# Performance work log

Hardware: AMD Instinct MI355X
Metric: run time of the kernel (lower is better)

The kernel has to match this reference:

```python
import jax, jax.numpy as jnp
import numpy as np

NUM_USERS = 200000
NUM_ITEMS = 100000
EMB = 64
NUM_LAYERS = 3


def setup_inputs() -> dict:
    rng = np.random.default_rng(0)
    E_INTER = 2_000_000
    # unique (user, item) interactions -> faithful to adj[e0, e1] = 1.0 set-semantics
    lin = np.unique(rng.integers(0, NUM_USERS * NUM_ITEMS, size=E_INTER, dtype=np.int64))
    u = (lin // NUM_ITEMS).astype(np.int32)
    it = (lin % NUM_ITEMS).astype(np.int32) + NUM_USERS  # item node ids offset by NUM_USERS
    row = np.concatenate([u, it])  # symmetric bipartite graph, no self-loops
    col = np.concatenate([it, u])
    edge_index = jnp.asarray(np.stack([row, col]), dtype=jnp.int32)  # [2, E]

    key = jax.random.key(0)
    k1, k2 = jax.random.split(key)
    # xavier_uniform on nn.Embedding.weight
    bu = float(np.sqrt(6.0 / (NUM_USERS + EMB)))
    bi = float(np.sqrt(6.0 / (NUM_ITEMS + EMB)))
    user_emb = jax.random.uniform(k1, (NUM_USERS, EMB), jnp.float32, -bu, bu)
    item_emb = jax.random.uniform(k2, (NUM_ITEMS, EMB), jnp.float32, -bi, bi)
    return {"edge_index": edge_index, "user_emb": user_emb, "item_emb": item_emb}


def reference(edge_index, user_emb, item_emb):
    num_users = user_emb.shape[0]
    N = num_users + item_emb.shape[0]
    x = jnp.concatenate([user_emb, item_emb], axis=0)  # ego embeddings [N, D]
    row, col = edge_index[0], edge_index[1]

    # adj has unique off-diagonal edges + eye(N): row-sum degree = edge count + 1
    deg = jax.ops.segment_sum(jnp.ones(row.shape, x.dtype), row, num_segments=N) + 1.0
    dinv = jax.lax.rsqrt(deg)                 # deg >= 1, never inf
    w = (dinv[row] * dinv[col])[:, None]      # per-edge D^-1/2 A D^-1/2 weight
    self_w = (dinv * dinv)[:, None]           # self-loop weight d_i^-1

    acc = x  # sum over layer outputs, including layer 0
    for _ in range(NUM_LAYERS):
        x = jax.ops.segment_sum(w * x[col], row, num_segments=N) + self_w * x
        # dropout is identity in eval mode
        acc = acc + x

    return acc[:num_users], acc[num_users:]
```

## Files before the change

### kernel.cpp

```cpp
#include <hip/hip_runtime.h>
#include <hip/hip_bf16.h>

#define EMB 64
#define BKT_BITS 10
#define BKT_SZ   (1 << BKT_BITS)
#define NBMAX    256
#define PAD      32
#define U_BITS   18
#define U_MASK   ((1u << U_BITS) - 1u)

__device__ __forceinline__ float bf2f(unsigned short h) {
    return __uint_as_float(((unsigned)h) << 16);
}
__device__ __forceinline__ unsigned short f2bf(float f) {
    unsigned u = __float_as_uint(f);
    unsigned r = (u + 0x7fffu + ((u >> 16) & 1u)) >> 16;
    return (unsigned short)r;
}

__global__ void k1_kernel(const int* __restrict__ row, const int* __restrict__ colh,
                          int* __restrict__ urp, float* __restrict__ dinv,
                          const float* __restrict__ ue, unsigned short* __restrict__ y0,
                          int* __restrict__ btotp,
                          int NU, int Eh, int NB, int UB) {
    __shared__ int bound[17];
    __shared__ int hist[NBMAX];
    int t = threadIdx.x;
    if ((int)blockIdx.x < UB) {
        int r0 = blockIdx.x * 16;
        if (t < 17) {
            int r = r0 + t;
            if (r <= NU) {
                int lo = 0, hi = Eh;
                while (lo < hi) {
                    int mid = (lo + hi) >> 1;
                    if (row[mid] < r) lo = mid + 1; else hi = mid;
                }
                bound[t] = lo;
                urp[r] = lo;
                if (t < 16 && r < NU)
                    dinv[r] = rsqrtf((float)(0) + 0.0f);
            }
        }
        __syncthreads();
        if (t < 16 && r0 + t < NU)
            dinv[r0 + t] = rsqrtf((float)(bound[t + 1] - bound[t]) + 1.0f);
        long j4 = (long)r0 * 64 + t * 4;
        if (j4 < (long)NU * 64) {
            int rb = t >> 4;
            float sc = rsqrtf((float)(bound[rb + 1] - bound[rb]) + 1.0f);
            float4 v = ((const float4*)ue)[j4 >> 2];
            ushort4 o;
            o.x = f2bf(sc * v.x); o.y = f2bf(sc * v.y);
            o.z = f2bf(sc * v.z); o.w = f2bf(sc * v.w);
            ((ushort4*)y0)[j4 >> 2] = o;
        }
    } else {
        hist[t] = 0;
        if (t + 256 < NBMAX) hist[t + 256] = 0;
        __syncthreads();
        long e0 = (long)(blockIdx.x - UB) * 4096;
#pragma unroll
        for (int k = 0; k < 16; ++k) {
            long e = e0 + k * 256 + t;
            if (e < Eh) atomicAdd(&hist[(colh[e] - NU) >> BKT_BITS], 1);
        }
        __syncthreads();
        if (t < NB && hist[t]) atomicAdd(&btotp[t * PAD], hist[t]);
    }
}

__global__ void scanS_kernel(const int* __restrict__ btotp, int* __restrict__ bbase,
                             int* __restrict__ bcurp, int NB, int Eh) {
    __shared__ int sh[256];
    int t = threadIdx.x;
    int v = (t < NB) ? btotp[t * PAD] : 0;
    sh[t] = v;
    __syncthreads();
    for (int off = 1; off < 256; off <<= 1) {
        int u = (t >= off) ? sh[t - off] : 0;
        __syncthreads();
        sh[t] += u;
        __syncthreads();
    }
    if (t < NB) {
        int excl = sh[t] - v;
        bbase[t] = excl;
        bcurp[t * PAD] = excl;
        if (t == NB - 1) bbase[NB] = sh[t];
    }
}

__global__ void passA_kernel(const int* __restrict__ rowh, const int* __restrict__ colh,
                             int* __restrict__ bcurp, unsigned* __restrict__ staging,
                             int Eh, int NU, int NB) {
    __shared__ int cnt[NBMAX];
    __shared__ int base[NBMAX];
    int t = threadIdx.x;
    cnt[t] = 0;
    if (t + 256 < NBMAX) cnt[t + 256] = 0;
    __syncthreads();
    long cb = (long)blockIdx.x * 1024;
    int b[4], rk[4];
    unsigned pk[4];
#pragma unroll
    for (int j = 0; j < 4; ++j) {
        long e = cb + j * 256 + t;
        if (e < Eh) {
            int u = rowh[e];
            int loc = colh[e] - NU;
            b[j] = loc >> BKT_BITS;
            pk[j] = ((unsigned)(loc & (BKT_SZ - 1)) << U_BITS) | (unsigned)u;
            rk[j] = atomicAdd(&cnt[b[j]], 1);
        } else {
            b[j] = -1;
        }
    }
    __syncthreads();
    if (t < NB) base[t] = cnt[t] ? atomicAdd(&bcurp[t * PAD], cnt[t]) : 0;
    __syncthreads();
#pragma unroll
    for (int j = 0; j < 4; ++j)
        if (b[j] >= 0) staging[base[b[j]] + rk[j]] = pk[j];
}

__global__ void passB_kernel(const unsigned* __restrict__ staging,
                             const int* __restrict__ bbase,
                             int* __restrict__ irp, int* __restrict__ icols,
                             float* __restrict__ dinv,
                             const float* __restrict__ ie, unsigned short* __restrict__ y0,
                             int NU, int NI, int NB, int Eh) {
    __shared__ int cnt[BKT_SZ];
    __shared__ int sh[BKT_SZ];
    int t = threadIdx.x;
    int b = blockIdx.x;
    int lo = b << BKT_BITS;
    int sb = bbase[b], se = bbase[b + 1];

    cnt[t] = 0;
    __syncthreads();
    for (int k = sb + t; k < se; k += 1024)
        atomicAdd(&cnt[staging[k] >> U_BITS], 1);
    __syncthreads();

    sh[t] = cnt[t];
    __syncthreads();
    for (int off = 1; off < 1024; off <<= 1) {
        int v = (t >= off) ? sh[t - off] : 0;
        __syncthreads();
        sh[t] += v;
        __syncthreads();
    }
    int exclv = sh[t] - cnt[t];
    int item = lo + t;
    if (item < NI) {
        irp[item] = sb + exclv;
        dinv[NU + item] = rsqrtf((float)cnt[t] + 1.0f);
    }
    if (b == NB - 1 && t == 0) irp[NI] = Eh;
    __syncthreads();
    sh[t] = exclv;
    __syncthreads();
    for (int k = sb + t; k < se; k += 1024) {
        unsigned v = staging[k];
        int io = (int)(v >> U_BITS);
        int r = atomicAdd(&sh[io], 1);
        icols[sb + r] = (int)(v & U_MASK);
    }

    for (int m = t; m < BKT_SZ * 16; m += 1024) {
        int it = lo + (m >> 4);
        if (it >= NI) break;
        float sc = rsqrtf((float)cnt[m >> 4] + 1.0f);
        float4 v = ((const float4*)ie)[(long)it * 16 + (m & 15)];
        ushort4 o;
        o.x = f2bf(sc * v.x); o.y = f2bf(sc * v.y);
        o.z = f2bf(sc * v.z); o.w = f2bf(sc * v.w);
        ((ushort4*)y0)[((long)NU + it) * 16 + (m & 15)] = o;
    }
}

__global__ void ul0_kernel(const int* __restrict__ urp, const int* __restrict__ colg,
                           const float* __restrict__ dinv,
                           const unsigned short* __restrict__ y0,
                           unsigned short* __restrict__ y1, int NU) {
    long t = (long)blockIdx.x * blockDim.x + threadIdx.x;
    int i = (int)(t >> 4);
    if (i >= NU) return;
    int q = (int)(t & 15);
    int s = urp[i], e = urp[i + 1];
    float di = dinv[i];
    const ushort4* __restrict__ y04 = (const ushort4*)y0;
    long p = (long)i * 16 + q;
    ushort4 sv = y04[p];

    float ax = 0.f, ay = 0.f, az = 0.f, aw = 0.f;
    for (int k0 = s; k0 < e; k0 += 8) {
        int   c[8];
        float w[8];
#pragma unroll
        for (int j = 0; j < 8; ++j) {
            int k = k0 + j;
            bool v = (k < e);
            c[j] = v ? colg[k] : 0;
            w[j] = v ? 1.0f : 0.0f;
        }
        ushort4 u[8];
#pragma unroll
        for (int j = 0; j < 8; ++j) u[j] = y04[(long)c[j] * 16 + q];
#pragma unroll
        for (int j = 0; j < 8; ++j) {
            ax += w[j] * bf2f(u[j].x);
            ay += w[j] * bf2f(u[j].y);
            az += w[j] * bf2f(u[j].z);
            aw += w[j] * bf2f(u[j].w);
        }
    }
    ax += bf2f(sv.x); ay += bf2f(sv.y); az += bf2f(sv.z); aw += bf2f(sv.w);
    float sq = di * di;
    ushort4 o;
    o.x = f2bf(sq * ax); o.y = f2bf(sq * ay); o.z = f2bf(sq * az); o.w = f2bf(sq * aw);
    ((ushort4*)y1)[p] = o;
}

__global__ void d2_kernel(const int* __restrict__ irp, const int* __restrict__ icols,
                          const float* __restrict__ dinv,
                          const unsigned short* __restrict__ y0,
                          unsigned short* __restrict__ y1,
                          unsigned short* __restrict__ y2, int NU, int NI) {
    long t = (long)blockIdx.x * blockDim.x + threadIdx.x;
    int j = (int)(t >> 4);
    if (j >= NI) return;
    int q = (int)(t & 15);
    int i = NU + j;
    int s = irp[j], e = irp[j + 1];
    float di = dinv[i];
    const ushort4* __restrict__ y04 = (const ushort4*)y0;
    const ushort4* __restrict__ y14 = (const ushort4*)y1;
    long p = (long)i * 16 + q;
    ushort4 sv0 = y04[p];

    float a0x = 0.f, a0y = 0.f, a0z = 0.f, a0w = 0.f;
    float a1x = 0.f, a1y = 0.f, a1z = 0.f, a1w = 0.f;
    for (int k0 = s; k0 < e; k0 += 8) {
        long  off[8];
        float w[8];
#pragma unroll
        for (int jj = 0; jj < 8; ++jj) {
            int k = k0 + jj;
            bool v = (k < e);
            int c = v ? icols[k] : 0;
            off[jj] = (long)c * 16 + q;
            w[jj] = v ? 1.0f : 0.0f;
        }
        ushort4 u0[8], u1[8];
#pragma unroll
        for (int jj = 0; jj < 8; ++jj) { u0[jj] = y04[off[jj]]; u1[jj] = y14[off[jj]]; }
#pragma unroll
        for (int jj = 0; jj < 8; ++jj) {
            a0x += w[jj] * bf2f(u0[jj].x); a0y += w[jj] * bf2f(u0[jj].y);
            a0z += w[jj] * bf2f(u0[jj].z); a0w += w[jj] * bf2f(u0[jj].w);
            a1x += w[jj] * bf2f(u1[jj].x); a1y += w[jj] * bf2f(u1[jj].y);
            a1z += w[jj] * bf2f(u1[jj].z); a1w += w[jj] * bf2f(u1[jj].w);
        }
    }
    float sq = di * di;
    a0x += bf2f(sv0.x); a0y += bf2f(sv0.y); a0z += bf2f(sv0.z); a0w += bf2f(sv0.w);
    ushort4 o1;
    o1.x = f2bf(sq * a0x); o1.y = f2bf(sq * a0y);
    o1.z = f2bf(sq * a0z); o1.w = f2bf(sq * a0w);
    ((ushort4*)y1)[p] = o1;
    a1x += bf2f(o1.x); a1y += bf2f(o1.y); a1z += bf2f(o1.z); a1w += bf2f(o1.w);
    ushort4 o2;
    o2.x = f2bf(sq * a1x); o2.y = f2bf(sq * a1y);
    o2.z = f2bf(sq * a1z); o2.w = f2bf(sq * a1w);
    ((ushort4*)y2)[p] = o2;
}

__global__ void d3_kernel(const int* __restrict__ urp, const int* __restrict__ colg,
                          const float* __restrict__ dinv,
                          const unsigned short* __restrict__ y0,
                          const unsigned short* __restrict__ y1,
                          unsigned short* __restrict__ y2,
                          float* __restrict__ out, int NU) {
    long t = (long)blockIdx.x * blockDim.x + threadIdx.x;
    int i = (int)(t >> 4);
    if (i >= NU) return;
    int q = (int)(t & 15);
    int s = urp[i], e = urp[i + 1];
    float di = dinv[i];
    const ushort4* __restrict__ y04 = (const ushort4*)y0;
    const ushort4* __restrict__ y14 = (const ushort4*)y1;
    const ushort4* __restrict__ y24 = (const ushort4*)y2;
    long p = (long)i * 16 + q;
    ushort4 sv0 = y04[p];
    ushort4 sv1 = y14[p];

    float a1x = 0.f, a1y = 0.f, a1z = 0.f, a1w = 0.f;
    float a2x = 0.f, a2y = 0.f, a2z = 0.f, a2w = 0.f;
    for (int k0 = s; k0 < e; k0 += 8) {
        long  off[8];
        float w[8];
#pragma unroll
        for (int jj = 0; jj < 8; ++jj) {
            int k = k0 + jj;
            bool v = (k < e);
            int c = v ? colg[k] : 0;
            off[jj] = (long)c * 16 + q;
            w[jj] = v ? 1.0f : 0.0f;
        }
        ushort4 u1[8], u2[8];
#pragma unroll
        for (int jj = 0; jj < 8; ++jj) { u1[jj] = y14[off[jj]]; u2[jj] = y24[off[jj]]; }
#pragma unroll
        for (int jj = 0; jj < 8; ++jj) {
            a1x += w[jj] * bf2f(u1[jj].x); a1y += w[jj] * bf2f(u1[jj].y);
            a1z += w[jj] * bf2f(u1[jj].z); a1w += w[jj] * bf2f(u1[jj].w);
            a2x += w[jj] * bf2f(u2[jj].x); a2y += w[jj] * bf2f(u2[jj].y);
            a2z += w[jj] * bf2f(u2[jj].z); a2w += w[jj] * bf2f(u2[jj].w);
        }
    }
    float sq = di * di;
    a1x += bf2f(sv1.x); a1y += bf2f(sv1.y); a1z += bf2f(sv1.z); a1w += bf2f(sv1.w);
    ushort4 o2;
    o2.x = f2bf(sq * a1x); o2.y = f2bf(sq * a1y);
    o2.z = f2bf(sq * a1z); o2.w = f2bf(sq * a1w);
    ((ushort4*)y2)[p] = o2;
    a2x += bf2f(o2.x); a2y += bf2f(o2.y); a2z += bf2f(o2.z); a2w += bf2f(o2.w);
    float inv = 1.0f / di;
    float4 o;
    o.x = (bf2f(sv0.x) + bf2f(sv1.x) + bf2f(o2.x)) * inv + di * a2x;
    o.y = (bf2f(sv0.y) + bf2f(sv1.y) + bf2f(o2.y)) * inv + di * a2y;
    o.z = (bf2f(sv0.z) + bf2f(sv1.z) + bf2f(o2.z)) * inv + di * a2z;
    o.w = (bf2f(sv0.w) + bf2f(sv1.w) + bf2f(o2.w)) * inv + di * a2w;
    ((float4*)out)[p] = o;
}

__global__ void d4_kernel(const int* __restrict__ irp, const int* __restrict__ icols,
                          const float* __restrict__ dinv,
                          const unsigned short* __restrict__ y0,
                          const unsigned short* __restrict__ y1,
                          const unsigned short* __restrict__ y2,
                          float* __restrict__ out, int NU, int NI) {
    long t = (long)blockIdx.x * blockDim.x + threadIdx.x;
    int j = (int)(t >> 4);
    if (j >= NI) return;
    int q = (int)(t & 15);
    int i = NU + j;
    int s = irp[j], e = irp[j + 1];
    float di = dinv[i];
    const ushort4* __restrict__ y04 = (const ushort4*)y0;
    const ushort4* __restrict__ y14 = (const ushort4*)y1;
    const ushort4* __restrict__ y24 = (const ushort4*)y2;
    long p = (long)i * 16 + q;
    ushort4 sv0 = y04[p];
    ushort4 sv1 = y14[p];
    ushort4 sv2 = y24[p];

    float ax = 0.f, ay = 0.f, az = 0.f, aw = 0.f;
    for (int k0 = s; k0 < e; k0 += 8) {
        int   c[8];
        float w[8];
#pragma unroll
        for (int jj = 0; jj < 8; ++jj) {
            int k = k0 + jj;
            bool v = (k < e);
            c[jj] = v ? icols[k] : 0;
            w[jj] = v ? 1.0f : 0.0f;
        }
        ushort4 u[8];
#pragma unroll
        for (int jj = 0; jj < 8; ++jj) u[jj] = y24[(long)c[jj] * 16 + q];
#pragma unroll
        for (int jj = 0; jj < 8; ++jj) {
            ax += w[jj] * bf2f(u[jj].x);
            ay += w[jj] * bf2f(u[jj].y);
            az += w[jj] * bf2f(u[jj].z);
            aw += w[jj] * bf2f(u[jj].w);
        }
    }
    ax += bf2f(sv2.x); ay += bf2f(sv2.y); az += bf2f(sv2.z); aw += bf2f(sv2.w);
    float inv = 1.0f / di;
    float4 o;
    o.x = (bf2f(sv0.x) + bf2f(sv1.x) + bf2f(sv2.x)) * inv + di * ax;
    o.y = (bf2f(sv0.y) + bf2f(sv1.y) + bf2f(sv2.y)) * inv + di * ay;
    o.z = (bf2f(sv0.z) + bf2f(sv1.z) + bf2f(sv2.z)) * inv + di * az;
    o.w = (bf2f(sv0.w) + bf2f(sv1.w) + bf2f(sv2.w)) * inv + di * aw;
    ((float4*)out)[p] = o;
}

extern "C" void kernel_launch(void* const* d_in, const int* in_sizes, int n_in,
                              void* d_out, int out_size, void* d_ws, size_t ws_size,
                              hipStream_t stream) {
    const int*   edge_index = (const int*)d_in[0];
    const float* user_emb   = (const float*)d_in[1];
    const float* item_emb   = (const float*)d_in[2];
    float* out = (float*)d_out;

    const int  E  = in_sizes[0] / 2;
    const int  Eh = E / 2;
    const int  NU = in_sizes[1] / EMB;
    const int  NI = in_sizes[2] / EMB;
    const int  N  = NU + NI;
    const long total = (long)N * EMB;

    const int* row = edge_index;
    const int* col = edge_index + E;
    const int* rowh = row;
    const int* colh = col;

    int*   urp   = (int*)d_ws;
    int*   btotp = urp + (NU + 1);
    int*   bcurp = btotp + NBMAX * PAD;
    int*   bbase = bcurp + NBMAX * PAD;
    int*   irp   = bbase + (NBMAX + 1);
    int*   icols = irp + (NI + 1);
    float* dinv  = (float*)(icols + Eh);
    unsigned short* y0 = (unsigned short*)(((uintptr_t)(dinv + N) + 127) & ~(uintptr_t)127);
    unsigned short* y1 = y0 + total;
    unsigned short* y2 = y1 + total;
    unsigned* staging = (unsigned*)(y1 + (long)NU * EMB);

    const int NB = (NI + BKT_SZ - 1) >> BKT_BITS;

    hipMemsetAsync(btotp, 0, (size_t)NBMAX * PAD * sizeof(int), stream);

    int UB = (NU + 15) / 16;
    int PC = (Eh + 4095) / 4096;
    k1_kernel<<<UB + PC, 256, 0, stream>>>(row, colh, urp, dinv, user_emb, y0,
                                           btotp, NU, Eh, NB, UB);

    scanS_kernel<<<1, 256, 0, stream>>>(btotp, bbase, bcurp, NB, Eh);

    passA_kernel<<<(Eh + 1023) / 1024, 256, 0, stream>>>(rowh, colh, bcurp, staging,
                                                         Eh, NU, NB);

    passB_kernel<<<NB, 1024, 0, stream>>>(staging, bbase, irp, icols, dinv,
                                          item_emb, y0, NU, NI, NB, Eh);

    int nb_us = (int)(((long)NU * 16 + 255) / 256);
    ul0_kernel<<<nb_us, 256, 0, stream>>>(urp, col, dinv, y0, y1, NU);

    int nb_it = (int)(((long)NI * 16 + 255) / 256);
    d2_kernel<<<nb_it, 256, 0, stream>>>(irp, icols, dinv, y0, y1, y2, NU, NI);

    d3_kernel<<<nb_us, 256, 0, stream>>>(urp, col, dinv, y0, y1, y2, out, NU);

    d4_kernel<<<nb_it, 256, 0, stream>>>(irp, icols, dinv, y0, y1, y2, out, NU, NI);
}
```

Measured before the change: 531.9 us.

## Interleave paired layer embeddings so each neighbor gather fetches one 16-byte vector

Changes the bf16 embedding buffers to an interleaved layout. User layer-0 and layer-1 rows are stored side by side, and so are item layer-1 and layer-2 rows. The d2 and d3 gathers can then fetch both needed layers for a neighbor with one uint4 load instead of two separate 8-byte loads. The aim is fewer gather transactions and better cache-line use in the memory-bound sparse aggregation. The cost is more complex indexing, and the layer-0 user writes and layer-1 reads now use strided half-lines.

```diff
diff --git a/kernel.cpp b/kernel.cpp
--- a/kernel.cpp
+++ b/kernel.cpp
@@ -17,10 +17,15 @@
     unsigned r = (u + 0x7fffu + ((u >> 16) & 1u)) >> 16;
     return (unsigned short)r;
 }
+__device__ __forceinline__ float bflo(unsigned p) { return __uint_as_float(p << 16); }
+__device__ __forceinline__ float bfhi(unsigned p) { return __uint_as_float(p & 0xffff0000u); }
+__device__ __forceinline__ unsigned pack2(float a, float b) {
+    return (unsigned)f2bf(a) | ((unsigned)f2bf(b) << 16);
+}
 
 __global__ void k1_kernel(const int* __restrict__ row, const int* __restrict__ colh,
                           int* __restrict__ urp, float* __restrict__ dinv,
-                          const float* __restrict__ ue, unsigned short* __restrict__ y0,
+                          const float* __restrict__ ue, unsigned short* __restrict__ yu01,
                           int* __restrict__ btotp,
                           int NU, int Eh, int NB, int UB) {
     __shared__ int bound[17];
@@ -38,8 +43,6 @@
                 }
                 bound[t] = lo;
                 urp[r] = lo;
-                if (t < 16 && r < NU)
-                    dinv[r] = rsqrtf((float)(0) + 0.0f);
             }
         }
         __syncthreads();
@@ -48,16 +51,16 @@
         long j4 = (long)r0 * 64 + t * 4;
         if (j4 < (long)NU * 64) {
             int rb = t >> 4;
+            int q  = t & 15;
             float sc = rsqrtf((float)(bound[rb + 1] - bound[rb]) + 1.0f);
             float4 v = ((const float4*)ue)[j4 >> 2];
             ushort4 o;
             o.x = f2bf(sc * v.x); o.y = f2bf(sc * v.y);
             o.z = f2bf(sc * v.z); o.w = f2bf(sc * v.w);
-            ((ushort4*)y0)[j4 >> 2] = o;
+            ((ushort4*)yu01)[((long)(r0 + rb) * 16 + q) * 2 + 0] = o;
         }
     } else {
         hist[t] = 0;
-        if (t + 256 < NBMAX) hist[t + 256] = 0;
         __syncthreads();
         long e0 = (long)(blockIdx.x - UB) * 4096;
 #pragma unroll
@@ -98,7 +101,6 @@
     __shared__ int base[NBMAX];
     int t = threadIdx.x;
     cnt[t] = 0;
-    if (t + 256 < NBMAX) cnt[t + 256] = 0;
     __syncthreads();
     long cb = (long)blockIdx.x * 1024;
     int b[4], rk[4];
@@ -128,7 +130,7 @@
                              const int* __restrict__ bbase,
                              int* __restrict__ irp, int* __restrict__ icols,
                              float* __restrict__ dinv,
-                             const float* __restrict__ ie, unsigned short* __restrict__ y0,
+                             const float* __restrict__ ie, unsigned short* __restrict__ y0i,
                              int NU, int NI, int NB, int Eh) {
     __shared__ int cnt[BKT_SZ];
     __shared__ int sh[BKT_SZ];
@@ -176,23 +178,22 @@
         ushort4 o;
         o.x = f2bf(sc * v.x); o.y = f2bf(sc * v.y);
         o.z = f2bf(sc * v.z); o.w = f2bf(sc * v.w);
-        ((ushort4*)y0)[((long)NU + it) * 16 + (m & 15)] = o;
+        ((ushort4*)y0i)[(long)it * 16 + (m & 15)] = o;
     }
 }
 
 __global__ void ul0_kernel(const int* __restrict__ urp, const int* __restrict__ colg,
                            const float* __restrict__ dinv,
-                           const unsigned short* __restrict__ y0,
-                           unsigned short* __restrict__ y1, int NU) {
+                           const unsigned short* __restrict__ y0i,
+                           unsigned short* __restrict__ yu01, int NU) {
     long t = (long)blockIdx.x * blockDim.x + threadIdx.x;
     int i = (int)(t >> 4);
     if (i >= NU) return;
     int q = (int)(t & 15);
     int s = urp[i], e = urp[i + 1];
     float di = dinv[i];
-    const ushort4* __restrict__ y04 = (const ushort4*)y0;
-    long p = (long)i * 16 + q;
-    ushort4 sv = y04[p];
+    const ushort4* __restrict__ y0is = (const ushort4*)y0i - (long)NU * 16;
+    ushort4 sv = ((const ushort4*)yu01)[((long)i * 16 + q) * 2 + 0];
 
     float ax = 0.f, ay = 0.f, az = 0.f, aw = 0.f;
     for (int k0 = s; k0 < e; k0 += 8) {
@@ -202,12 +203,12 @@
         for (int j = 0; j < 8; ++j) {
             int k = k0 + j;
             bool v = (k < e);
-            c[j] = v ? colg[k] : 0;
+            c[j] = v ? colg[k] : NU;
             w[j] = v ? 1.0f : 0.0f;
         }
         ushort4 u[8];
 #pragma unroll
-        for (int j = 0; j < 8; ++j) u[j] = y04[(long)c[j] * 16 + q];
+        for (int j = 0; j < 8; ++j) u[j] = y0is[(long)c[j] * 16 + q];
 #pragma unroll
         for (int j = 0; j < 8; ++j) {
             ax += w[j] * bf2f(u[j].x);
@@ -220,68 +221,63 @@
     float sq = di * di;
     ushort4 o;
     o.x = f2bf(sq * ax); o.y = f2bf(sq * ay); o.z = f2bf(sq * az); o.w = f2bf(sq * aw);
-    ((ushort4*)y1)[p] = o;
+    ((ushort4*)yu01)[((long)i * 16 + q) * 2 + 1] = o;
 }
 
 __global__ void d2_kernel(const int* __restrict__ irp, const int* __restrict__ icols,
                           const float* __restrict__ dinv,
-                          const unsigned short* __restrict__ y0,
-                          unsigned short* __restrict__ y1,
-                          unsigned short* __restrict__ y2, int NU, int NI) {
+                          const unsigned short* __restrict__ yu01,
+                          const unsigned short* __restrict__ y0i,
+                          unsigned short* __restrict__ yi12, int NU, int NI) {
     long t = (long)blockIdx.x * blockDim.x + threadIdx.x;
     int j = (int)(t >> 4);
     if (j >= NI) return;
     int q = (int)(t & 15);
-    int i = NU + j;
     int s = irp[j], e = irp[j + 1];
-    float di = dinv[i];
-    const ushort4* __restrict__ y04 = (const ushort4*)y0;
-    const ushort4* __restrict__ y14 = (const ushort4*)y1;
-    long p = (long)i * 16 + q;
-    ushort4 sv0 = y04[p];
+    float di = dinv[NU + j];
+    const uint4* __restrict__ yu = (const uint4*)yu01;
+    ushort4 sv0 = ((const ushort4*)y0i)[(long)j * 16 + q];
 
     float a0x = 0.f, a0y = 0.f, a0z = 0.f, a0w = 0.f;
     float a1x = 0.f, a1y = 0.f, a1z = 0.f, a1w = 0.f;
     for (int k0 = s; k0 < e; k0 += 8) {
-        long  off[8];
+        int   off[8];
         float w[8];
 #pragma unroll
         for (int jj = 0; jj < 8; ++jj) {
             int k = k0 + jj;
             bool v = (k < e);
             int c = v ? icols[k] : 0;
-            off[jj] = (long)c * 16 + q;
+            off[jj] = c * 16 + q;
             w[jj] = v ? 1.0f : 0.0f;
         }
-        ushort4 u0[8], u1[8];
-#pragma unroll
-        for (int jj = 0; jj < 8; ++jj) { u0[jj] = y04[off[jj]]; u1[jj] = y14[off[jj]]; }
-#pragma unroll
-        for (int jj = 0; jj < 8; ++jj) {
-            a0x += w[jj] * bf2f(u0[jj].x); a0y += w[jj] * bf2f(u0[jj].y);
-            a0z += w[jj] * bf2f(u0[jj].z); a0w += w[jj] * bf2f(u0[jj].w);
-            a1x += w[jj] * bf2f(u1[jj].x); a1y += w[jj] * bf2f(u1[jj].y);
-            a1z += w[jj] * bf2f(u1[jj].z); a1w += w[jj] * bf2f(u1[jj].w);
+        uint4 u[8];
+#pragma unroll
+        for (int jj = 0; jj < 8; ++jj) u[jj] = yu[off[jj]];
+#pragma unroll
+        for (int jj = 0; jj < 8; ++jj) {
+            a0x += w[jj] * bflo(u[jj].x); a0y += w[jj] * bfhi(u[jj].x);
+            a0z += w[jj] * bflo(u[jj].y); a0w += w[jj] * bfhi(u[jj].y);
+            a1x += w[jj] * bflo(u[jj].z); a1y += w[jj] * bfhi(u[jj].z);
+            a1z += w[jj] * bflo(u[jj].w); a1w += w[jj] * bfhi(u[jj].w);
         }
     }
     float sq = di * di;
     a0x += bf2f(sv0.x); a0y += bf2f(sv0.y); a0z += bf2f(sv0.z); a0w += bf2f(sv0.w);
-    ushort4 o1;
-    o1.x = f2bf(sq * a0x); o1.y = f2bf(sq * a0y);
-    o1.z = f2bf(sq * a0z); o1.w = f2bf(sq * a0w);
-    ((ushort4*)y1)[p] = o1;
-    a1x += bf2f(o1.x); a1y += bf2f(o1.y); a1z += bf2f(o1.z); a1w += bf2f(o1.w);
-    ushort4 o2;
-    o2.x = f2bf(sq * a1x); o2.y = f2bf(sq * a1y);
-    o2.z = f2bf(sq * a1z); o2.w = f2bf(sq * a1w);
-    ((ushort4*)y2)[p] = o2;
+    unsigned o1x = pack2(sq * a0x, sq * a0y);
+    unsigned o1y = pack2(sq * a0z, sq * a0w);
+    a1x += bflo(o1x); a1y += bfhi(o1x); a1z += bflo(o1y); a1w += bfhi(o1y);
+    unsigned o2x = pack2(sq * a1x, sq * a1y);
+    unsigned o2y = pack2(sq * a1z, sq * a1w);
+    uint4 o; o.x = o1x; o.y = o1y; o.z = o2x; o.w = o2y;
+    ((uint4*)yi12)[(long)j * 16 + q] = o;
 }
 
 __global__ void d3_kernel(const int* __restrict__ urp, const int* __restrict__ colg,
                           const float* __restrict__ dinv,
-                          const unsigned short* __restrict__ y0,
-                          const unsigned short* __restrict__ y1,
-                          unsigned short* __restrict__ y2,
+                          const unsigned short* __restrict__ yu01,
+                          const unsigned short* __restrict__ yi12,
+                          unsigned short* __restrict__ y2u,
                           float* __restrict__ out, int NU) {
     long t = (long)blockIdx.x * blockDim.x + threadIdx.x;
     int i = (int)(t >> 4);
@@ -289,73 +285,63 @@
     int q = (int)(t & 15);
     int s = urp[i], e = urp[i + 1];
     float di = dinv[i];
-    const ushort4* __restrict__ y04 = (const ushort4*)y0;
-    const ushort4* __restrict__ y14 = (const ushort4*)y1;
-    const ushort4* __restrict__ y24 = (const ushort4*)y2;
-    long p = (long)i * 16 + q;
-    ushort4 sv0 = y04[p];
-    ushort4 sv1 = y14[p];
+    const uint4* __restrict__ yis = (const uint4*)yi12 - (long)NU * 16;
+    uint4 su = ((const uint4*)yu01)[(long)i * 16 + q];
 
     float a1x = 0.f, a1y = 0.f, a1z = 0.f, a1w = 0.f;
     float a2x = 0.f, a2y = 0.f, a2z = 0.f, a2w = 0.f;
     for (int k0 = s; k0 < e; k0 += 8) {
-        long  off[8];
+        int   off[8];
         float w[8];
 #pragma unroll
         for (int jj = 0; jj < 8; ++jj) {
             int k = k0 + jj;
             bool v = (k < e);
-            int c = v ? colg[k] : 0;
-            off[jj] = (long)c * 16 + q;
+            int c = v ? colg[k] : NU;
+            off[jj] = c * 16 + q;
             w[jj] = v ? 1.0f : 0.0f;
         }
-        ushort4 u1[8], u2[8];
-#pragma unroll
-        for (int jj = 0; jj < 8; ++jj) { u1[jj] = y14[off[jj]]; u2[jj] = y24[off[jj]]; }
-#pragma unroll
-        for (int jj = 0; jj < 8; ++jj) {
-            a1x += w[jj] * bf2f(u1[jj].x); a1y += w[jj] * bf2f(u1[jj].y);
-            a1z += w[jj] * bf2f(u1[jj].z); a1w += w[jj] * bf2f(u1[jj].w);
-            a2x += w[jj] * bf2f(u2[jj].x); a2y += w[jj] * bf2f(u2[jj].y);
-            a2z += w[jj] * bf2f(u2[jj].z); a2w += w[jj] * bf2f(u2[jj].w);
+        uint4 u[8];
+#pragma unroll
+        for (int jj = 0; jj < 8; ++jj) u[jj] = yis[(long)off[jj]];
+#pragma unroll
+        for (int jj = 0; jj < 8; ++jj) {
+            a1x += w[jj] * bflo(u[jj].x); a1y += w[jj] * bfhi(u[jj].x);
+            a1z += w[jj] * bflo(u[jj].y); a1w += w[jj] * bfhi(u[jj].y);
+            a2x += w[jj] * bflo(u[jj].z); a2y += w[jj] * bfhi(u[jj].z);
+            a2z += w[jj] * bflo(u[jj].w); a2w += w[jj] * bfhi(u[jj].w);
         }
     }
     float sq = di * di;
-    a1x += bf2f(sv1.x); a1y += bf2f(sv1.y); a1z += bf2f(sv1.z); a1w += bf2f(sv1.w);
-    ushort4 o2;
-    o2.x = f2bf(sq * a1x); o2.y = f2bf(sq * a1y);
-    o2.z = f2bf(sq * a1z); o2.w = f2bf(sq * a1w);
-    ((ushort4*)y2)[p] = o2;
-    a2x += bf2f(o2.x); a2y += bf2f(o2.y); a2z += bf2f(o2.z); a2w += bf2f(o2.w);
+    a1x += bflo(su.z); a1y += bfhi(su.z); a1z += bflo(su.w); a1w += bfhi(su.w);
+    unsigned o2x = pack2(sq * a1x, sq * a1y);
+    unsigned o2y = pack2(sq * a1z, sq * a1w);
+    ((uint2*)y2u)[(long)i * 16 + q] = make_uint2(o2x, o2y);
+    a2x += bflo(o2x); a2y += bfhi(o2x); a2z += bflo(o2y); a2w += bfhi(o2y);
     float inv = 1.0f / di;
     float4 o;
-    o.x = (bf2f(sv0.x) + bf2f(sv1.x) + bf2f(o2.x)) * inv + di * a2x;
-    o.y = (bf2f(sv0.y) + bf2f(sv1.y) + bf2f(o2.y)) * inv + di * a2y;
-    o.z = (bf2f(sv0.z) + bf2f(sv1.z) + bf2f(o2.z)) * inv + di * a2z;
-    o.w = (bf2f(sv0.w) + bf2f(sv1.w) + bf2f(o2.w)) * inv + di * a2w;
-    ((float4*)out)[p] = o;
+    o.x = (bflo(su.x) + bflo(su.z) + bflo(o2x)) * inv + di * a2x;
+    o.y = (bfhi(su.x) + bfhi(su.z) + bfhi(o2x)) * inv + di * a2y;
+    o.z = (bflo(su.y) + bflo(su.w) + bflo(o2y)) * inv + di * a2z;
+    o.w = (bfhi(su.y) + bfhi(su.w) + bfhi(o2y)) * inv + di * a2w;
+    ((float4*)out)[(long)i * 16 + q] = o;
 }
 
 __global__ void d4_kernel(const int* __restrict__ irp, const int* __restrict__ icols,
                           const float* __restrict__ dinv,
-                          const unsigned short* __restrict__ y0,
-                          const unsigned short* __restrict__ y1,
-                          const unsigned short* __restrict__ y2,
+                          const unsigned short* __restrict__ y0i,
+                          const unsigned short* __restrict__ yi12,
+                          const unsigned short* __restrict__ y2u,
                           float* __restrict__ out, int NU, int NI) {
     long t = (long)blockIdx.x * blockDim.x + threadIdx.x;
     int j = (int)(t >> 4);
     if (j >= NI) return;
     int q = (int)(t & 15);
-    int i = NU + j;
     int s = irp[j], e = irp[j + 1];
-    float di = dinv[i];
-    const ushort4* __restrict__ y04 = (const ushort4*)y0;
-    const ushort4* __restrict__ y14 = (const ushort4*)y1;
-    const ushort4* __restrict__ y24 = (const ushort4*)y2;
-    long p = (long)i * 16 + q;
-    ushort4 sv0 = y04[p];
-    ushort4 sv1 = y14[p];
-    ushort4 sv2 = y24[p];
+    float di = dinv[NU + j];
+    const ushort4* __restrict__ y2u4 = (const ushort4*)y2u;
+    ushort4 sv0 = ((const ushort4*)y0i)[(long)j * 16 + q];
+    uint4   si  = ((const uint4*)yi12)[(long)j * 16 + q];
 
     float ax = 0.f, ay = 0.f, az = 0.f, aw = 0.f;
     for (int k0 = s; k0 < e; k0 += 8) {
@@ -370,7 +356,7 @@
         }
         ushort4 u[8];
 #pragma unroll
-        for (int jj = 0; jj < 8; ++jj) u[jj] = y24[(long)c[jj] * 16 + q];
+        for (int jj = 0; jj < 8; ++jj) u[jj] = y2u4[(long)c[jj] * 16 + q];
 #pragma unroll
         for (int jj = 0; jj < 8; ++jj) {
             ax += w[jj] * bf2f(u[jj].x);
@@ -379,14 +365,14 @@
             aw += w[jj] * bf2f(u[jj].w);
         }
     }
-    ax += bf2f(sv2.x); ay += bf2f(sv2.y); az += bf2f(sv2.z); aw += bf2f(sv2.w);
+    ax += bflo(si.z); ay += bfhi(si.z); az += bflo(si.w); aw += bfhi(si.w);
     float inv = 1.0f / di;
     float4 o;
-    o.x = (bf2f(sv0.x) + bf2f(sv1.x) + bf2f(sv2.x)) * inv + di * ax;
-    o.y = (bf2f(sv0.y) + bf2f(sv1.y) + bf2f(sv2.y)) * inv + di * ay;
-    o.z = (bf2f(sv0.z) + bf2f(sv1.z) + bf2f(sv2.z)) * inv + di * az;
-    o.w = (bf2f(sv0.w) + bf2f(sv1.w) + bf2f(sv2.w)) * inv + di * aw;
-    ((float4*)out)[p] = o;
+    o.x = (bf2f(sv0.x) + bflo(si.x) + bflo(si.z)) * inv + di * ax;
+    o.y = (bf2f(sv0.y) + bfhi(si.x) + bfhi(si.z)) * inv + di * ay;
+    o.z = (bf2f(sv0.z) + bflo(si.y) + bflo(si.w)) * inv + di * az;
+    o.w = (bf2f(sv0.w) + bfhi(si.y) + bfhi(si.w)) * inv + di * aw;
+    ((float4*)out)[((long)NU + j) * 16 + q] = o;
 }
 
 extern "C" void kernel_launch(void* const* d_in, const int* in_sizes, int n_in,
@@ -402,24 +388,24 @@
     const int  NU = in_sizes[1] / EMB;
     const int  NI = in_sizes[2] / EMB;
     const int  N  = NU + NI;
-    const long total = (long)N * EMB;
 
     const int* row = edge_index;
     const int* col = edge_index + E;
     const int* rowh = row;
     const int* colh = col;
 
-    int*   urp   = (int*)d_ws;
-    int*   btotp = urp + (NU + 1);
-    int*   bcurp = btotp + NBMAX * PAD;
-    int*   bbase = bcurp + NBMAX * PAD;
-    int*   irp   = bbase + (NBMAX + 1);
-    int*   icols = irp + (NI + 1);
-    float* dinv  = (float*)(icols + Eh);
-    unsigned short* y0 = (unsigned short*)(((uintptr_t)(dinv + N) + 127) & ~(uintptr_t)127);
-    unsigned short* y1 = y0 + total;
-    unsigned short* y2 = y1 + total;
-    unsigned* staging = (unsigned*)(y1 + (long)NU * EMB);
+    int*   urp     = (int*)d_ws;
+    int*   btotp   = urp + (NU + 1);
+    int*   bcurp   = btotp + NBMAX * PAD;
+    int*   bbase   = bcurp + NBMAX * PAD;
+    int*   irp     = bbase + (NBMAX + 1);
+    int*   icols   = irp + (NI + 1);
+    unsigned* staging = (unsigned*)(icols + Eh);
+    float* dinv    = (float*)(staging + Eh);
+    unsigned short* yu01 = (unsigned short*)(((uintptr_t)(dinv + N) + 127) & ~(uintptr_t)127);
+    unsigned short* y0i  = yu01 + (long)NU * 128;
+    unsigned short* yi12 = y0i + (long)NI * 64;
+    unsigned short* y2u  = yi12 + (long)NI * 128;
 
     const int NB = (NI + BKT_SZ - 1) >> BKT_BITS;
 
@@ -427,7 +413,7 @@
 
     int UB = (NU + 15) / 16;
     int PC = (Eh + 4095) / 4096;
-    k1_kernel<<<UB + PC, 256, 0, stream>>>(row, colh, urp, dinv, user_emb, y0,
+    k1_kernel<<<UB + PC, 256, 0, stream>>>(row, colh, urp, dinv, user_emb, yu01,
                                            btotp, NU, Eh, NB, UB);
 
     scanS_kernel<<<1, 256, 0, stream>>>(btotp, bbase, bcurp, NB, Eh);
@@ -436,15 +422,15 @@
                                                          Eh, NU, NB);
 
     passB_kernel<<<NB, 1024, 0, stream>>>(staging, bbase, irp, icols, dinv,
-                                          item_emb, y0, NU, NI, NB, Eh);
+                                          item_emb, y0i, NU, NI, NB, Eh);
 
     int nb_us = (int)(((long)NU * 16 + 255) / 256);
-    ul0_kernel<<<nb_us, 256, 0, stream>>>(urp, col, dinv, y0, y1, NU);
+    ul0_kernel<<<nb_us, 256, 0, stream>>>(urp, col, dinv, y0i, yu01, NU);
 
     int nb_it = (int)(((long)NI * 16 + 255) / 256);
-    d2_kernel<<<nb_it, 256, 0, stream>>>(irp, icols, dinv, y0, y1, y2, NU, NI);
-
-    d3_kernel<<<nb_us, 256, 0, stream>>>(urp, col, dinv, y0, y1, y2, out, NU);
-
-    d4_kernel<<<nb_it, 256, 0, stream>>>(irp, icols, dinv, y0, y1, y2, out, NU, NI);
-}
+    d2_kernel<<<nb_it, 256, 0, stream>>>(irp, icols, dinv, yu01, y0i, yi12, NU, NI);
+
+    d3_kernel<<<nb_us, 256, 0, stream>>>(urp, col, dinv, yu01, yi12, y2u, out, NU);
+
+    d4_kernel<<<nb_it, 256, 0, stream>>>(irp, icols, dinv, y0i, yi12, y2u, out, NU, NI);
+}
```

New measurement: 530.0 us. About the same (-0.4%).
